# Kernel optimization log

Measured on AMD Instinct MI355X. Metric: run time of the kernel, lower is better.

## Reference

```python
import jax, jax.numpy as jnp
import numpy as np

N_EMBD = 1024
HEAD_SIZE = 64


def setup_inputs() -> dict:
    key = jax.random.key(0)
    ks = jax.random.split(key, 7)
    B, T, C, H = 4, 4096, N_EMBD, HEAD_SIZE
    s = 1.0 / np.sqrt(C)
    return {
        "x": jax.random.normal(ks[0], (B, T, C), dtype=jnp.float32),
        "Wk": jax.random.uniform(ks[1], (C, H), jnp.float32, -s, s),
        "bk": jax.random.uniform(ks[2], (H,), jnp.float32, -s, s),
        "Wq": jax.random.uniform(ks[3], (C, H), jnp.float32, -s, s),
        "bq": jax.random.uniform(ks[4], (H,), jnp.float32, -s, s),
        "Wv": jax.random.uniform(ks[5], (C, H), jnp.float32, -s, s),
        "bv": jax.random.uniform(ks[6], (H,), jnp.float32, -s, s),
    }


def reference(x, Wk, bk, Wq, bq, Wv, bv):
    B, T, C = x.shape
    k = x @ Wk + bk  # [B,T,H]
    q = x @ Wq + bq
    v = x @ Wv + bv
    scale = k.shape[-1] ** -0.5
    wei = jnp.einsum("bth,bsh->bts", q, k) * scale  # [B,T,T]
    causal = jnp.tril(jnp.ones((T, T), dtype=bool))
    wei = jnp.where(causal, wei, -jnp.inf)
    wei = jax.nn.softmax(wei, axis=-1)
    return jnp.einsum("bts,bsh->bth", wei, v)
```

## Files before the change

### kernel.cpp

```cpp
#include <hip/hip_runtime.h>
#include <hip/hip_bf16.h>


typedef _Float16 f16;
typedef f16 half4 __attribute__((ext_vector_type(4)));
typedef f16 half8 __attribute__((ext_vector_type(8)));
typedef float f32x4 __attribute__((ext_vector_type(4)));

#define T_SEQ 4096
#define QSCL 0.1803368801111204f

__device__ __forceinline__ f32x4 mfma16(half8 a, half8 b, f32x4 c) {
    return __builtin_amdgcn_mfma_f32_16x16x32_f16(a, b, c, 0, 0, 0);
}

__global__ __launch_bounds__(256) void prep_w(const float* __restrict__ Wq,
                                              const float* __restrict__ Wk,
                                              const float* __restrict__ Wv,
                                              f16* __restrict__ Wfrag) {
    int nt = blockIdx.x;
    int mat = nt >> 2;
    const float* W = (mat == 0) ? Wq : (mat == 1 ? Wk : Wv);
    float s = (mat == 0) ? QSCL : 1.0f;
    int tid = threadIdx.x;
    int lane = tid & 63, g = lane >> 4, c16 = lane & 15;
    int ksb = (tid >> 6) * 8;
    int h = ((nt & 3) << 4) + c16;
#pragma unroll
    for (int q = 0; q < 8; ++q) {
        int ks = ksb + q;
        half8 o;
#pragma unroll
        for (int j = 0; j < 8; ++j) {
            int k = ks * 32 + g * 8 + j;
            o[j] = (f16)(W[(size_t)k * 64 + h] * s);
        }
        *reinterpret_cast<half8*>(&Wfrag[((size_t)(nt * 32 + ks) * 64 + lane) * 8]) = o;
    }
}

__global__ __launch_bounds__(256, 4) void proj(const float* __restrict__ x,
                                               const f16* __restrict__ Wfrag,
                                               const float* __restrict__ bk,
                                               const float* __restrict__ bq,
                                               const float* __restrict__ bv,
                                               f16* __restrict__ Qb, f16* __restrict__ Kb,
                                               f16* __restrict__ Vbt) {
    __shared__ f16 xs[16][1032];
    int m0 = blockIdx.x << 4;
    int tid = threadIdx.x;
    int w = tid >> 6, lane = tid & 63, g = lane >> 4, c16 = lane & 15;
    {
        int row = tid >> 4;
        int c0 = (tid & 15) << 2;
        const float* xr = &x[(size_t)(m0 + row) * 1024 + c0];
#pragma unroll
        for (int chunk = 0; chunk < 8; ++chunk) {
            float4 A = *reinterpret_cast<const float4*>(xr + chunk * 128);
            float4 B = *reinterpret_cast<const float4*>(xr + chunk * 128 + 64);
            half4 ha, hb;
            ha[0] = (f16)A.x; ha[1] = (f16)A.y; ha[2] = (f16)A.z; ha[3] = (f16)A.w;
            hb[0] = (f16)B.x; hb[1] = (f16)B.y; hb[2] = (f16)B.z; hb[3] = (f16)B.w;
            *reinterpret_cast<half4*>(&xs[row][c0 + chunk * 128]) = ha;
            *reinterpret_cast<half4*>(&xs[row][c0 + chunk * 128 + 64]) = hb;
        }
    }
    __syncthreads();
    f32x4 zero = {0.f, 0.f, 0.f, 0.f};
    f32x4 acc[3];
#pragma unroll
    for (int i = 0; i < 3; ++i) acc[i] = zero;
    const f16* wbase = &Wfrag[(size_t)(w * 3) * 32 * 64 * 8 + (size_t)lane * 8];
#pragma unroll 8
    for (int ks = 0; ks < 32; ++ks) {
        half8 a = *reinterpret_cast<const half8*>(&xs[c16][ks * 32 + g * 8]);
#pragma unroll
        for (int i = 0; i < 3; ++i) {
            half8 bf = *reinterpret_cast<const half8*>(
                wbase + ((size_t)i * 32 + ks) * 64 * 8);
            acc[i] = mfma16(a, bf, acc[i]);
        }
    }
    int b = m0 >> 12;
#pragma unroll
    for (int i = 0; i < 3; ++i) {
        int nt = w * 3 + i;
        int mat = nt >> 2;
        int h = ((nt & 3) << 4) + c16;
        float bias = (mat == 0) ? bq[h] * QSCL : (mat == 1 ? bk[h] : bv[h]);
#pragma unroll
        for (int j = 0; j < 4; ++j) {
            int row = m0 + g * 4 + j;
            f16 val = (f16)(acc[i][j] + bias);
            if (mat == 0) Qb[(size_t)row * 64 + h] = val;
            else if (mat == 1) Kb[(size_t)row * 64 + h] = val;
            else Vbt[((size_t)(b * 64 + h)) * 4096 + (row & 4095)] = val;
        }
    }
}

__global__ __launch_bounds__(256) void attn(const f16* __restrict__ Qb,
                                            const f16* __restrict__ Kb,
                                            const f16* __restrict__ Vbt,
                                            f16* __restrict__ Opart,
                                            float* __restrict__ Ml) {
    int qt = 63 - blockIdx.x;
    int b = blockIdx.y, ck = blockIdx.z;
    int t0 = ck << 4;
    if (t0 > qt) return;
    int nT = min(t0 + 16, qt + 1);
    int nIter = nT - t0;
    int q0 = qt << 6;
    const f16* Q = Qb + (size_t)b * T_SEQ * 64;
    const f16* K = Kb + (size_t)b * T_SEQ * 64;
    const f16* Vg = Vbt + (size_t)b * 64 * T_SEQ;
    int tid = threadIdx.x;
    int w = tid >> 6, lane = tid & 63, g = lane >> 4, c16 = lane & 15;
    __shared__ f16 Kt[2][64][72];
    __shared__ f16 Vt[2][64][72];
    __shared__ f16 Pl[4][16][72];

    half8 qf0 = *reinterpret_cast<const half8*>(&Q[(size_t)(q0 + 16 * w + c16) * 64 + g * 8]);
    half8 qf1 = *reinterpret_cast<const half8*>(&Q[(size_t)(q0 + 16 * w + c16) * 64 + 32 + g * 8]);

    f32x4 zero = {0.f, 0.f, 0.f, 0.f};
    f32x4 oacc[4];
#pragma unroll
    for (int i = 0; i < 4; ++i) oacc[i] = zero;
    float m_run = -__builtin_inff(), l_run = 0.f;

    int sr = tid >> 2, sc = (tid & 3) << 4;
    int k0 = t0 << 6;
    half8 kr0 = *reinterpret_cast<const half8*>(&K[(size_t)(k0 + sr) * 64 + sc]);
    half8 kr1 = *reinterpret_cast<const half8*>(&K[(size_t)(k0 + sr) * 64 + sc + 8]);
    half8 vr0 = *reinterpret_cast<const half8*>(&Vg[(size_t)sr * T_SEQ + k0 + sc]);
    half8 vr1 = *reinterpret_cast<const half8*>(&Vg[(size_t)sr * T_SEQ + k0 + sc + 8]);
    *reinterpret_cast<half8*>(&Kt[0][sr][sc]) = kr0;
    *reinterpret_cast<half8*>(&Kt[0][sr][sc + 8]) = kr1;
    *reinterpret_cast<half8*>(&Vt[0][sr][sc]) = vr0;
    *reinterpret_cast<half8*>(&Vt[0][sr][sc + 8]) = vr1;
    __syncthreads();
    int cur = 0;

    for (int it = 0; it < nIter; ++it) {
        int gt = t0 + it;
        if (it + 1 < nIter) {
            int kn = (gt + 1) << 6;
            kr0 = *reinterpret_cast<const half8*>(&K[(size_t)(kn + sr) * 64 + sc]);
            kr1 = *reinterpret_cast<const half8*>(&K[(size_t)(kn + sr) * 64 + sc + 8]);
            vr0 = *reinterpret_cast<const half8*>(&Vg[(size_t)sr * T_SEQ + kn + sc]);
            vr1 = *reinterpret_cast<const half8*>(&Vg[(size_t)sr * T_SEQ + kn + sc + 8]);
        }
        f32x4 st[4];
#pragma unroll
        for (int nt = 0; nt < 4; ++nt) st[nt] = zero;
#pragma unroll
        for (int nt = 0; nt < 4; ++nt) {
            half8 kf0 = *reinterpret_cast<const half8*>(&Kt[cur][nt * 16 + c16][g * 8]);
            half8 kf1 = *reinterpret_cast<const half8*>(&Kt[cur][nt * 16 + c16][32 + g * 8]);
            st[nt] = mfma16(kf0, qf0, st[nt]);
            st[nt] = mfma16(kf1, qf1, st[nt]);
        }
        if (gt == qt) {
            int kb = gt << 6;
            int qr = q0 + 16 * w + c16;
#pragma unroll
            for (int nt = 0; nt < 4; ++nt)
#pragma unroll
                for (int jj = 0; jj < 4; ++jj)
                    if (kb + nt * 16 + g * 4 + jj > qr) st[nt][jj] = -1e30f;
        }
        float m01, m23, mx;
        {
            f32x4 a = st[0], bq4 = st[1], c = st[2], d = st[3];
            f32x4 e;
            e[0] = fmaxf(fmaxf(a[0], a[1]), fmaxf(a[2], a[3]));
            e[1] = fmaxf(fmaxf(bq4[0], bq4[1]), fmaxf(bq4[2], bq4[3]));
            e[2] = fmaxf(fmaxf(c[0], c[1]), fmaxf(c[2], c[3]));
            e[3] = fmaxf(fmaxf(d[0], d[1]), fmaxf(d[2], d[3]));
            m01 = fmaxf(e[0], e[1]); m23 = fmaxf(e[2], e[3]);
            mx = fmaxf(m01, m23);
        }
        mx = fmaxf(mx, __shfl_xor(mx, 16, 64));
        mx = fmaxf(mx, __shfl_xor(mx, 32, 64));
        float nm = fmaxf(m_run, mx);
        float al = exp2f(m_run - nm);
        m_run = nm;
        float pm[4][4];
        float rs = 0.f;
#pragma unroll
        for (int nt = 0; nt < 4; ++nt) {
            float s0 = exp2f(st[nt][0] - m_run);
            float s1 = exp2f(st[nt][1] - m_run);
            float s2 = exp2f(st[nt][2] - m_run);
            float s3 = exp2f(st[nt][3] - m_run);
            pm[nt][0] = s0; pm[nt][1] = s1; pm[nt][2] = s2; pm[nt][3] = s3;
            rs += (s0 + s1) + (s2 + s3);
        }
        rs += __shfl_xor(rs, 16, 64);
        rs += __shfl_xor(rs, 32, 64);
        l_run = l_run * al + rs;
#pragma unroll
        for (int ht = 0; ht < 4; ++ht)
#pragma unroll
            for (int jj = 0; jj < 4; ++jj) oacc[ht][jj] *= al;
#pragma unroll
        for (int nt = 0; nt < 4; ++nt) {
            half4 p4;
            p4[0] = (f16)pm[nt][0]; p4[1] = (f16)pm[nt][1];
            p4[2] = (f16)pm[nt][2]; p4[3] = (f16)pm[nt][3];
            *reinterpret_cast<half4*>(&Pl[w][c16][nt * 16 + g * 4]) = p4;
        }
        half8 pa0 = *reinterpret_cast<const half8*>(&Pl[w][c16][g * 8]);
        half8 pa1 = *reinterpret_cast<const half8*>(&Pl[w][c16][32 + g * 8]);
#pragma unroll
        for (int ht = 0; ht < 4; ++ht) {
            half8 vb0 = *reinterpret_cast<const half8*>(&Vt[cur][ht * 16 + c16][g * 8]);
            half8 vb1 = *reinterpret_cast<const half8*>(&Vt[cur][ht * 16 + c16][32 + g * 8]);
            oacc[ht] = mfma16(vb0, pa0, oacc[ht]);
            oacc[ht] = mfma16(vb1, pa1, oacc[ht]);
        }
        if (it + 1 < nIter) {
            *reinterpret_cast<half8*>(&Kt[cur ^ 1][sr][sc]) = kr0;
            *reinterpret_cast<half8*>(&Kt[cur ^ 1][sr][sc + 8]) = kr1;
            *reinterpret_cast<half8*>(&Vt[cur ^ 1][sr][sc]) = vr0;
            *reinterpret_cast<half8*>(&Vt[cur ^ 1][sr][sc + 8]) = vr1;
        }
        __syncthreads();
        cur ^= 1;
    }
    int slot = (((b << 6) + qt) << 2) + ck;
    f16* Op = Opart + (size_t)slot * 4096;
    float* mlp = Ml + (size_t)slot * 128;
    int r = 16 * w + c16;
#pragma unroll
    for (int ht = 0; ht < 4; ++ht) {
        half4 o4;
        o4[0] = (f16)oacc[ht][0]; o4[1] = (f16)oacc[ht][1];
        o4[2] = (f16)oacc[ht][2]; o4[3] = (f16)oacc[ht][3];
        *reinterpret_cast<half4*>(&Op[r * 64 + ht * 16 + g * 4]) = o4;
    }
    if (g == 0) { mlp[r] = m_run; mlp[64 + r] = l_run; }
}

__global__ __launch_bounds__(256) void combine(const f16* __restrict__ Opart,
                                               const float* __restrict__ Ml,
                                               float* __restrict__ out) {
    int qt = blockIdx.x, b = blockIdx.y;
    int nck = (qt >> 4) + 1;
    int tid = threadIdx.x;
    int row = tid >> 2, c0 = (tid & 3) << 4;
    int bslot = ((b << 6) + qt) << 2;
    float mv[4], lv[4];
    float M = -1e30f;
#pragma unroll
    for (int i = 0; i < 4; ++i)
        if (i < nck) {
            mv[i] = Ml[(size_t)(bslot + i) * 128 + row];
            lv[i] = Ml[(size_t)(bslot + i) * 128 + 64 + row];
            M = fmaxf(M, mv[i]);
        }
    float L = 0.f, sc[4];
#pragma unroll
    for (int i = 0; i < 4; ++i)
        if (i < nck) { sc[i] = exp2f(mv[i] - M); L += lv[i] * sc[i]; }
    float inv = 1.0f / L;
    float o[16];
#pragma unroll
    for (int j = 0; j < 16; ++j) o[j] = 0.f;
#pragma unroll
    for (int i = 0; i < 4; ++i)
        if (i < nck) {
            const f16* Op = Opart + (size_t)(bslot + i) * 4096 + row * 64 + c0;
            half8 h0 = *reinterpret_cast<const half8*>(Op);
            half8 h1 = *reinterpret_cast<const half8*>(Op + 8);
#pragma unroll
            for (int j = 0; j < 8; ++j) {
                o[j] += sc[i] * (float)h0[j];
                o[8 + j] += sc[i] * (float)h1[j];
            }
        }
    float* op = &out[((size_t)b * T_SEQ + (qt << 6) + row) * 64 + c0];
#pragma unroll
    for (int j = 0; j < 16; ++j) op[j] = o[j] * inv;
}

extern "C" void kernel_launch(void* const* d_in, const int* in_sizes, int n_in,
                              void* d_out, int out_size, void* d_ws, size_t ws_size,
                              hipStream_t stream) {
    (void)in_sizes; (void)n_in; (void)out_size; (void)ws_size;
    const float* x  = (const float*)d_in[0];
    const float* Wk = (const float*)d_in[1];
    const float* bk = (const float*)d_in[2];
    const float* Wq = (const float*)d_in[3];
    const float* bq = (const float*)d_in[4];
    const float* Wv = (const float*)d_in[5];
    const float* bv = (const float*)d_in[6];
    float* out = (float*)d_out;
    char* ws = (char*)d_ws;
    f16* Wfrag = (f16*)(ws);
    f16* Qb    = (f16*)(ws + 393216);
    f16* Kb    = (f16*)(ws + 393216 + 2097152);
    f16* Vbt   = (f16*)(ws + 393216 + 2 * 2097152);
    f16* Opart = (f16*)(ws + 393216 + 3 * 2097152);
    float* Ml  = (float*)(ws + 393216 + 3 * 2097152 + 8388608);

    prep_w<<<12, 256, 0, stream>>>(Wq, Wk, Wv, Wfrag);
    proj<<<1024, 256, 0, stream>>>(x, Wfrag, bk, bq, bv, Qb, Kb, Vbt);
    attn<<<dim3(64, 4, 4), 256, 0, stream>>>(Qb, Kb, Vbt, Opart, Ml);
    combine<<<dim3(64, 4), 256, 0, stream>>>(Opart, Ml, out);
}
```

Before: 159.2 us.

## Process two key tiles per iteration and compact attention grid to live blocks

```diff
diff --git a/kernel.cpp b/kernel.cpp
--- a/kernel.cpp
+++ b/kernel.cpp
@@ -104,12 +104,16 @@
                                             const f16* __restrict__ Vbt,
                                             f16* __restrict__ Opart,
                                             float* __restrict__ Ml) {
-    int qt = 63 - blockIdx.x;
-    int b = blockIdx.y, ck = blockIdx.z;
-    int t0 = ck << 4;
-    if (t0 > qt) return;
-    int nT = min(t0 + 16, qt + 1);
-    int nIter = nT - t0;
+    int idx = 159 - (int)blockIdx.x;
+    int qt, ck;
+    if (idx < 16) { qt = idx; ck = 0; }
+    else if (idx < 48) { int j = idx - 16; qt = 16 + (j >> 1); ck = j & 1; }
+    else if (idx < 96) { int j = idx - 48; int q3 = j / 3; qt = 32 + q3; ck = j - 3 * q3; }
+    else { int j = idx - 96; qt = 48 + (j >> 2); ck = j & 3; }
+    int b = blockIdx.y;
+    int nT = min(16, qt + 1 - (ck << 4));
+    int npairs = (nT + 1) >> 1;
+    int kend = ((ck << 4) + nT) << 6;
     int q0 = qt << 6;
     const f16* Q = Qb + (size_t)b * T_SEQ * 64;
     const f16* K = Kb + (size_t)b * T_SEQ * 64;
@@ -118,10 +122,11 @@
     int w = tid >> 6, lane = tid & 63, g = lane >> 4, c16 = lane & 15;
     __shared__ f16 Kt[2][64][72];
     __shared__ f16 Vt[2][64][72];
-    __shared__ f16 Pl[4][16][72];
-
-    half8 qf0 = *reinterpret_cast<const half8*>(&Q[(size_t)(q0 + 16 * w + c16) * 64 + g * 8]);
-    half8 qf1 = *reinterpret_cast<const half8*>(&Q[(size_t)(q0 + 16 * w + c16) * 64 + 32 + g * 8]);
+    __shared__ f16 Pl[4][16][136];
+
+    int qr = q0 + 16 * w + c16;
+    half8 qf0 = *reinterpret_cast<const half8*>(&Q[(size_t)qr * 64 + g * 8]);
+    half8 qf1 = *reinterpret_cast<const half8*>(&Q[(size_t)qr * 64 + 32 + g * 8]);
 
     f32x4 zero = {0.f, 0.f, 0.f, 0.f};
     f32x4 oacc[4];
@@ -130,71 +135,88 @@
     float m_run = -__builtin_inff(), l_run = 0.f;
 
     int sr = tid >> 2, sc = (tid & 3) << 4;
-    int k0 = t0 << 6;
-    half8 kr0 = *reinterpret_cast<const half8*>(&K[(size_t)(k0 + sr) * 64 + sc]);
-    half8 kr1 = *reinterpret_cast<const half8*>(&K[(size_t)(k0 + sr) * 64 + sc + 8]);
-    half8 vr0 = *reinterpret_cast<const half8*>(&Vg[(size_t)sr * T_SEQ + k0 + sc]);
-    half8 vr1 = *reinterpret_cast<const half8*>(&Vg[(size_t)sr * T_SEQ + k0 + sc + 8]);
-    *reinterpret_cast<half8*>(&Kt[0][sr][sc]) = kr0;
-    *reinterpret_cast<half8*>(&Kt[0][sr][sc + 8]) = kr1;
-    *reinterpret_cast<half8*>(&Vt[0][sr][sc]) = vr0;
-    *reinterpret_cast<half8*>(&Vt[0][sr][sc + 8]) = vr1;
+    int kb0 = ck << 10;
+    half8 k00, k01, k10, k11, v00, v01, v10, v11;
+    {
+        const f16* Kp = &K[(size_t)(kb0 + sr) * 64 + sc];
+        k00 = *reinterpret_cast<const half8*>(Kp);
+        k01 = *reinterpret_cast<const half8*>(Kp + 8);
+        k10 = *reinterpret_cast<const half8*>(Kp + 64 * 64);
+        k11 = *reinterpret_cast<const half8*>(Kp + 64 * 64 + 8);
+        const f16* Vp = &Vg[(size_t)sr * T_SEQ + kb0 + sc];
+        v00 = *reinterpret_cast<const half8*>(Vp);
+        v01 = *reinterpret_cast<const half8*>(Vp + 8);
+        v10 = *reinterpret_cast<const half8*>(Vp + 64);
+        v11 = *reinterpret_cast<const half8*>(Vp + 64 + 8);
+    }
+    *reinterpret_cast<half8*>(&Kt[0][sr][sc]) = k00;
+    *reinterpret_cast<half8*>(&Kt[0][sr][sc + 8]) = k01;
+    *reinterpret_cast<half8*>(&Kt[1][sr][sc]) = k10;
+    *reinterpret_cast<half8*>(&Kt[1][sr][sc + 8]) = k11;
+    *reinterpret_cast<half8*>(&Vt[0][sr][sc]) = v00;
+    *reinterpret_cast<half8*>(&Vt[0][sr][sc + 8]) = v01;
+    *reinterpret_cast<half8*>(&Vt[1][sr][sc]) = v10;
+    *reinterpret_cast<half8*>(&Vt[1][sr][sc + 8]) = v11;
     __syncthreads();
-    int cur = 0;
-
-    for (int it = 0; it < nIter; ++it) {
-        int gt = t0 + it;
-        if (it + 1 < nIter) {
-            int kn = (gt + 1) << 6;
-            kr0 = *reinterpret_cast<const half8*>(&K[(size_t)(kn + sr) * 64 + sc]);
-            kr1 = *reinterpret_cast<const half8*>(&K[(size_t)(kn + sr) * 64 + sc + 8]);
-            vr0 = *reinterpret_cast<const half8*>(&Vg[(size_t)sr * T_SEQ + kn + sc]);
-            vr1 = *reinterpret_cast<const half8*>(&Vg[(size_t)sr * T_SEQ + kn + sc + 8]);
-        }
-        f32x4 st[4];
-#pragma unroll
-        for (int nt = 0; nt < 4; ++nt) st[nt] = zero;
-#pragma unroll
-        for (int nt = 0; nt < 4; ++nt) {
-            half8 kf0 = *reinterpret_cast<const half8*>(&Kt[cur][nt * 16 + c16][g * 8]);
-            half8 kf1 = *reinterpret_cast<const half8*>(&Kt[cur][nt * 16 + c16][32 + g * 8]);
+
+    for (int p = 0; p < npairs; ++p) {
+        bool pre = (p + 1 < npairs);
+        if (pre) {
+            int kb2 = (ck << 10) + ((p + 1) << 7);
+            const f16* Kp = &K[(size_t)(kb2 + sr) * 64 + sc];
+            k00 = *reinterpret_cast<const half8*>(Kp);
+            k01 = *reinterpret_cast<const half8*>(Kp + 8);
+            k10 = *reinterpret_cast<const half8*>(Kp + 64 * 64);
+            k11 = *reinterpret_cast<const half8*>(Kp + 64 * 64 + 8);
+            const f16* Vp = &Vg[(size_t)sr * T_SEQ + kb2 + sc];
+            v00 = *reinterpret_cast<const half8*>(Vp);
+            v01 = *reinterpret_cast<const half8*>(Vp + 8);
+            v10 = *reinterpret_cast<const half8*>(Vp + 64);
+            v11 = *reinterpret_cast<const half8*>(Vp + 64 + 8);
+        }
+        f32x4 st[8];
+#pragma unroll
+        for (int nt = 0; nt < 8; ++nt) st[nt] = zero;
+#pragma unroll
+        for (int nt = 0; nt < 8; ++nt) {
+            const f16* kr = &Kt[nt >> 2][((nt & 3) << 4) + c16][0];
+            half8 kf0 = *reinterpret_cast<const half8*>(kr + g * 8);
+            half8 kf1 = *reinterpret_cast<const half8*>(kr + 32 + g * 8);
             st[nt] = mfma16(kf0, qf0, st[nt]);
             st[nt] = mfma16(kf1, qf1, st[nt]);
         }
-        if (gt == qt) {
-            int kb = gt << 6;
-            int qr = q0 + 16 * w + c16;
-#pragma unroll
-            for (int nt = 0; nt < 4; ++nt)
+        if (p == npairs - 1) {
+            int kbp = (ck << 10) + (p << 7);
+            int keylim = min(qr, kend - 1);
+#pragma unroll
+            for (int nt = 0; nt < 8; ++nt)
 #pragma unroll
                 for (int jj = 0; jj < 4; ++jj)
-                    if (kb + nt * 16 + g * 4 + jj > qr) st[nt][jj] = -1e30f;
-        }
-        float m01, m23, mx;
+                    if (kbp + nt * 16 + g * 4 + jj > keylim) st[nt][jj] = -1e30f;
+        }
+        float mx;
         {
-            f32x4 a = st[0], bq4 = st[1], c = st[2], d = st[3];
-            f32x4 e;
-            e[0] = fmaxf(fmaxf(a[0], a[1]), fmaxf(a[2], a[3]));
-            e[1] = fmaxf(fmaxf(bq4[0], bq4[1]), fmaxf(bq4[2], bq4[3]));
-            e[2] = fmaxf(fmaxf(c[0], c[1]), fmaxf(c[2], c[3]));
-            e[3] = fmaxf(fmaxf(d[0], d[1]), fmaxf(d[2], d[3]));
-            m01 = fmaxf(e[0], e[1]); m23 = fmaxf(e[2], e[3]);
-            mx = fmaxf(m01, m23);
+            f32x4 e01 = __builtin_elementwise_max(st[0], st[1]);
+            f32x4 e23 = __builtin_elementwise_max(st[2], st[3]);
+            f32x4 e45 = __builtin_elementwise_max(st[4], st[5]);
+            f32x4 e67 = __builtin_elementwise_max(st[6], st[7]);
+            f32x4 e = __builtin_elementwise_max(__builtin_elementwise_max(e01, e23),
+                                                __builtin_elementwise_max(e45, e67));
+            mx = fmaxf(fmaxf(e[0], e[1]), fmaxf(e[2], e[3]));
         }
         mx = fmaxf(mx, __shfl_xor(mx, 16, 64));
         mx = fmaxf(mx, __shfl_xor(mx, 32, 64));
         float nm = fmaxf(m_run, mx);
         float al = exp2f(m_run - nm);
         m_run = nm;
-        float pm[4][4];
         float rs = 0.f;
 #pragma unroll
-        for (int nt = 0; nt < 4; ++nt) {
+        for (int nt = 0; nt < 8; ++nt) {
             float s0 = exp2f(st[nt][0] - m_run);
             float s1 = exp2f(st[nt][1] - m_run);
             float s2 = exp2f(st[nt][2] - m_run);
             float s3 = exp2f(st[nt][3] - m_run);
-            pm[nt][0] = s0; pm[nt][1] = s1; pm[nt][2] = s2; pm[nt][3] = s3;
+            st[nt][0] = s0; st[nt][1] = s1; st[nt][2] = s2; st[nt][3] = s3;
             rs += (s0 + s1) + (s2 + s3);
         }
         rs += __shfl_xor(rs, 16, 64);
@@ -205,29 +227,34 @@
 #pragma unroll
             for (int jj = 0; jj < 4; ++jj) oacc[ht][jj] *= al;
 #pragma unroll
-        for (int nt = 0; nt < 4; ++nt) {
+        for (int nt = 0; nt < 8; ++nt) {
             half4 p4;
-            p4[0] = (f16)pm[nt][0]; p4[1] = (f16)pm[nt][1];
-            p4[2] = (f16)pm[nt][2]; p4[3] = (f16)pm[nt][3];
+            p4[0] = (f16)st[nt][0]; p4[1] = (f16)st[nt][1];
+            p4[2] = (f16)st[nt][2]; p4[3] = (f16)st[nt][3];
             *reinterpret_cast<half4*>(&Pl[w][c16][nt * 16 + g * 4]) = p4;
         }
-        half8 pa0 = *reinterpret_cast<const half8*>(&Pl[w][c16][g * 8]);
-        half8 pa1 = *reinterpret_cast<const half8*>(&Pl[w][c16][32 + g * 8]);
-#pragma unroll
-        for (int ht = 0; ht < 4; ++ht) {
-            half8 vb0 = *reinterpret_cast<const half8*>(&Vt[cur][ht * 16 + c16][g * 8]);
-            half8 vb1 = *reinterpret_cast<const half8*>(&Vt[cur][ht * 16 + c16][32 + g * 8]);
-            oacc[ht] = mfma16(vb0, pa0, oacc[ht]);
-            oacc[ht] = mfma16(vb1, pa1, oacc[ht]);
-        }
-        if (it + 1 < nIter) {
-            *reinterpret_cast<half8*>(&Kt[cur ^ 1][sr][sc]) = kr0;
-            *reinterpret_cast<half8*>(&Kt[cur ^ 1][sr][sc + 8]) = kr1;
-            *reinterpret_cast<half8*>(&Vt[cur ^ 1][sr][sc]) = vr0;
-            *reinterpret_cast<half8*>(&Vt[cur ^ 1][sr][sc + 8]) = vr1;
+#pragma unroll
+        for (int s = 0; s < 4; ++s) {
+            half8 pa = *reinterpret_cast<const half8*>(&Pl[w][c16][s * 32 + g * 8]);
+#pragma unroll
+            for (int ht = 0; ht < 4; ++ht) {
+                half8 vb = *reinterpret_cast<const half8*>(
+                    &Vt[s >> 1][ht * 16 + c16][(s & 1) * 32 + g * 8]);
+                oacc[ht] = mfma16(vb, pa, oacc[ht]);
+            }
         }
         __syncthreads();
-        cur ^= 1;
+        if (pre) {
+            *reinterpret_cast<half8*>(&Kt[0][sr][sc]) = k00;
+            *reinterpret_cast<half8*>(&Kt[0][sr][sc + 8]) = k01;
+            *reinterpret_cast<half8*>(&Kt[1][sr][sc]) = k10;
+            *reinterpret_cast<half8*>(&Kt[1][sr][sc + 8]) = k11;
+            *reinterpret_cast<half8*>(&Vt[0][sr][sc]) = v00;
+            *reinterpret_cast<half8*>(&Vt[0][sr][sc + 8]) = v01;
+            *reinterpret_cast<half8*>(&Vt[1][sr][sc]) = v10;
+            *reinterpret_cast<half8*>(&Vt[1][sr][sc + 8]) = v11;
+            __syncthreads();
+        }
     }
     int slot = (((b << 6) + qt) << 2) + ck;
     f16* Op = Opart + (size_t)slot * 4096;
@@ -307,6 +334,6 @@
 
     prep_w<<<12, 256, 0, stream>>>(Wq, Wk, Wv, Wfrag);
     proj<<<1024, 256, 0, stream>>>(x, Wfrag, bk, bq, bv, Qb, Kb, Vbt);
-    attn<<<dim3(64, 4, 4), 256, 0, stream>>>(Qb, Kb, Vbt, Opart, Ml);
+    attn<<<dim3(160, 4), 256, 0, stream>>>(Qb, Kb, Vbt, Opart, Ml);
     combine<<<dim3(64, 4), 256, 0, stream>>>(Opart, Ml, out);
 }
```

Result: slower. 164.5 us (+3.3%).

## Use compact 8-tile KV chunk grid with heaviest-first block mapping

Applied to the files above, without the earlier changes.

```diff
diff --git a/kernel.cpp b/kernel.cpp
--- a/kernel.cpp
+++ b/kernel.cpp
@@ -104,12 +104,16 @@
                                             const f16* __restrict__ Vbt,
                                             f16* __restrict__ Opart,
                                             float* __restrict__ Ml) {
-    int qt = 63 - blockIdx.x;
-    int b = blockIdx.y, ck = blockIdx.z;
-    int t0 = ck << 4;
-    if (t0 > qt) return;
-    int nT = min(t0 + 16, qt + 1);
-    int nIter = nT - t0;
+    int rem = 287 - (int)blockIdx.x;
+    int qt = 0, ck = 0;
+    for (int bd = 0; bd < 8; ++bd) {
+        int cnt = 8 * (bd + 1);
+        if (rem < cnt) { qt = bd * 8 + rem / (bd + 1); ck = rem % (bd + 1); break; }
+        rem -= cnt;
+    }
+    int b = blockIdx.y;
+    int t0 = ck << 3;
+    int nIter = min(8, qt + 1 - t0);
     int q0 = qt << 6;
     const f16* Q = Qb + (size_t)b * T_SEQ * 64;
     const f16* K = Kb + (size_t)b * T_SEQ * 64;
@@ -120,8 +124,9 @@
     __shared__ f16 Vt[2][64][72];
     __shared__ f16 Pl[4][16][72];
 
-    half8 qf0 = *reinterpret_cast<const half8*>(&Q[(size_t)(q0 + 16 * w + c16) * 64 + g * 8]);
-    half8 qf1 = *reinterpret_cast<const half8*>(&Q[(size_t)(q0 + 16 * w + c16) * 64 + 32 + g * 8]);
+    int qr = q0 + 16 * w + c16;
+    half8 qf0 = *reinterpret_cast<const half8*>(&Q[(size_t)qr * 64 + g * 8]);
+    half8 qf1 = *reinterpret_cast<const half8*>(&Q[(size_t)qr * 64 + 32 + g * 8]);
 
     f32x4 zero = {0.f, 0.f, 0.f, 0.f};
     f32x4 oacc[4];
@@ -163,30 +168,24 @@
         }
         if (gt == qt) {
             int kb = gt << 6;
-            int qr = q0 + 16 * w + c16;
 #pragma unroll
             for (int nt = 0; nt < 4; ++nt)
 #pragma unroll
                 for (int jj = 0; jj < 4; ++jj)
                     if (kb + nt * 16 + g * 4 + jj > qr) st[nt][jj] = -1e30f;
         }
-        float m01, m23, mx;
+        float mx;
         {
-            f32x4 a = st[0], bq4 = st[1], c = st[2], d = st[3];
-            f32x4 e;
-            e[0] = fmaxf(fmaxf(a[0], a[1]), fmaxf(a[2], a[3]));
-            e[1] = fmaxf(fmaxf(bq4[0], bq4[1]), fmaxf(bq4[2], bq4[3]));
-            e[2] = fmaxf(fmaxf(c[0], c[1]), fmaxf(c[2], c[3]));
-            e[3] = fmaxf(fmaxf(d[0], d[1]), fmaxf(d[2], d[3]));
-            m01 = fmaxf(e[0], e[1]); m23 = fmaxf(e[2], e[3]);
-            mx = fmaxf(m01, m23);
+            f32x4 e01 = __builtin_elementwise_max(st[0], st[1]);
+            f32x4 e23 = __builtin_elementwise_max(st[2], st[3]);
+            f32x4 e = __builtin_elementwise_max(e01, e23);
+            mx = fmaxf(fmaxf(e[0], e[1]), fmaxf(e[2], e[3]));
         }
         mx = fmaxf(mx, __shfl_xor(mx, 16, 64));
         mx = fmaxf(mx, __shfl_xor(mx, 32, 64));
         float nm = fmaxf(m_run, mx);
         float al = exp2f(m_run - nm);
         m_run = nm;
-        float pm[4][4];
         float rs = 0.f;
 #pragma unroll
         for (int nt = 0; nt < 4; ++nt) {
@@ -194,7 +193,7 @@
             float s1 = exp2f(st[nt][1] - m_run);
             float s2 = exp2f(st[nt][2] - m_run);
             float s3 = exp2f(st[nt][3] - m_run);
-            pm[nt][0] = s0; pm[nt][1] = s1; pm[nt][2] = s2; pm[nt][3] = s3;
+            st[nt][0] = s0; st[nt][1] = s1; st[nt][2] = s2; st[nt][3] = s3;
             rs += (s0 + s1) + (s2 + s3);
         }
         rs += __shfl_xor(rs, 16, 64);
@@ -207,8 +206,8 @@
 #pragma unroll
         for (int nt = 0; nt < 4; ++nt) {
             half4 p4;
-            p4[0] = (f16)pm[nt][0]; p4[1] = (f16)pm[nt][1];
-            p4[2] = (f16)pm[nt][2]; p4[3] = (f16)pm[nt][3];
+            p4[0] = (f16)st[nt][0]; p4[1] = (f16)st[nt][1];
+            p4[2] = (f16)st[nt][2]; p4[3] = (f16)st[nt][3];
             *reinterpret_cast<half4*>(&Pl[w][c16][nt * 16 + g * 4]) = p4;
         }
         half8 pa0 = *reinterpret_cast<const half8*>(&Pl[w][c16][g * 8]);
@@ -229,7 +228,7 @@
         __syncthreads();
         cur ^= 1;
     }
-    int slot = (((b << 6) + qt) << 2) + ck;
+    int slot = (((b << 6) + qt) << 3) + ck;
     f16* Op = Opart + (size_t)slot * 4096;
     float* mlp = Ml + (size_t)slot * 128;
     int r = 16 * w + c16;
@@ -247,29 +246,29 @@
                                                const float* __restrict__ Ml,
                                                float* __restrict__ out) {
     int qt = blockIdx.x, b = blockIdx.y;
-    int nck = (qt >> 4) + 1;
+    int nck = (qt >> 3) + 1;
     int tid = threadIdx.x;
     int row = tid >> 2, c0 = (tid & 3) << 4;
-    int bslot = ((b << 6) + qt) << 2;
-    float mv[4], lv[4];
+    int bslot = ((b << 6) + qt) << 3;
+    float mv[8], lv[8];
     float M = -1e30f;
 #pragma unroll
-    for (int i = 0; i < 4; ++i)
+    for (int i = 0; i < 8; ++i)
         if (i < nck) {
             mv[i] = Ml[(size_t)(bslot + i) * 128 + row];
             lv[i] = Ml[(size_t)(bslot + i) * 128 + 64 + row];
             M = fmaxf(M, mv[i]);
         }
-    float L = 0.f, sc[4];
-#pragma unroll
-    for (int i = 0; i < 4; ++i)
+    float L = 0.f, sc[8];
+#pragma unroll
+    for (int i = 0; i < 8; ++i)
         if (i < nck) { sc[i] = exp2f(mv[i] - M); L += lv[i] * sc[i]; }
     float inv = 1.0f / L;
     float o[16];
 #pragma unroll
     for (int j = 0; j < 16; ++j) o[j] = 0.f;
 #pragma unroll
-    for (int i = 0; i < 4; ++i)
+    for (int i = 0; i < 8; ++i)
         if (i < nck) {
             const f16* Op = Opart + (size_t)(bslot + i) * 4096 + row * 64 + c0;
             half8 h0 = *reinterpret_cast<const half8*>(Op);
@@ -303,10 +302,10 @@
     f16* Kb    = (f16*)(ws + 393216 + 2097152);
     f16* Vbt   = (f16*)(ws + 393216 + 2 * 2097152);
     f16* Opart = (f16*)(ws + 393216 + 3 * 2097152);
-    float* Ml  = (float*)(ws + 393216 + 3 * 2097152 + 8388608);
+    float* Ml  = (float*)(ws + 393216 + 3 * 2097152 + 16777216);
 
     prep_w<<<12, 256, 0, stream>>>(Wq, Wk, Wv, Wfrag);
     proj<<<1024, 256, 0, stream>>>(x, Wfrag, bk, bq, bv, Qb, Kb, Vbt);
-    attn<<<dim3(64, 4, 4), 256, 0, stream>>>(Qb, Kb, Vbt, Opart, Ml);
+    attn<<<dim3(288, 4), 256, 0, stream>>>(Qb, Kb, Vbt, Opart, Ml);
     combine<<<dim3(64, 4), 256, 0, stream>>>(Opart, Ml, out);
 }
```

After: 157.6 us. No clear change (-1.0%).
